# Optimization experiments

Hardware: AMD Instinct MI355X
Metric: run time of the kernel (lower is better)

The kernel has to match this reference:

```python
import jax, jax.numpy as jnp
import numpy as np

ANCHOR_LENGTHS = jnp.array([1., 2., 3., 4., 5., 7., 9.], dtype=jnp.float32)  # A = 7


def make_anchors_1d(Lf):
    # anchors [Lf*A, 2] in feature coords, matching torch make_anchors_1d
    centers = jnp.arange(Lf, dtype=jnp.float32) + 0.5          # [Lf]
    c = centers[:, None]                                        # [Lf,1]
    w = ANCHOR_LENGTHS[None, :]                                 # [1,A]
    start = c - 0.5 * w
    end = c + 0.5 * w
    return jnp.stack(jnp.broadcast_arrays(start, end), axis=-1).reshape(-1, 2)


def setup_inputs() -> dict:
    key = jax.random.key(0)
    ks = jax.random.split(key, 4)
    B, C, Lf, A = 8, 512, 16384, 7
    feat = jax.random.normal(ks[0], (B, C, Lf), dtype=jnp.float32)
    conv_w = jax.random.normal(ks[1], (C, C, 3), dtype=jnp.float32) * 0.02
    conv_b = jnp.zeros((C,), dtype=jnp.float32)
    obj_w = jax.random.normal(ks[2], (A, C, 1), dtype=jnp.float32) * 0.02
    obj_b = jnp.zeros((A,), dtype=jnp.float32)
    reg_w = jax.random.normal(ks[3], (A * 2, C, 1), dtype=jnp.float32) * 0.02
    reg_b = jnp.zeros((A * 2,), dtype=jnp.float32)
    return {"feat": feat, "conv_w": conv_w, "conv_b": conv_b,
            "obj_w": obj_w, "obj_b": obj_b, "reg_w": reg_w, "reg_b": reg_b}


def reference(feat, conv_w, conv_b, obj_w, obj_b, reg_w, reg_b):
    B, C, Lf = feat.shape
    A = obj_w.shape[0]
    # conv1d k=3 pad=1 (NCH layout), + bias, relu
    h = jax.lax.conv_general_dilated(
        feat, conv_w, window_strides=(1,), padding=((1, 1),),
        dimension_numbers=("NCH", "OIH", "NCH"))
    h = jax.nn.relu(h + conv_b[None, :, None])                  # [B,C,Lf]
    # 1x1 heads as channel contractions
    obj = jnp.einsum("bcl,ac->bla", h, obj_w[:, :, 0]) + obj_b  # [B,Lf,A]
    reg = jnp.einsum("bcl,oc->blo", h, reg_w[:, :, 0]) + reg_b  # [B,Lf,2A]
    obj = obj.reshape(B, Lf * A)                                # [B,N]
    reg = reg.reshape(B, Lf, A, 2).reshape(B, Lf * A, 2)        # [B,N,2]
    anchors = make_anchors_1d(Lf)                               # [N,2]
    return obj, reg, anchors
```

## Files before the change

### kernel.cpp

```cpp
#include <hip/hip_runtime.h>
#include <hip/hip_bf16.h>
#include <stdint.h>

typedef __attribute__((ext_vector_type(4))) float f32x4;
typedef unsigned short u16;
typedef unsigned int u32;
typedef unsigned char u8;

#define B_    8
#define C_    512
#define LF    16384
#define KTOT  1536

#define P4_BYTES ((size_t)4 * B_ * 21 * LF * 4)
#define W8_OFF   P4_BYTES

#define OBJ_OFF  0
#define REG_OFF  917504
#define ANC_OFF  2752512

__device__ __forceinline__ u16 f2bf(float f) {
    u32 u = __float_as_uint(f);
    return (u16)((u + 0x7FFFu + ((u >> 16) & 1u)) >> 16);
}
__device__ __forceinline__ u32 pk2bf(float lo, float hi) {
    u32 r;
    asm("v_cvt_pk_bf16_f32 %0, %1, %2" : "=v"(r) : "v"(lo), "v"(hi));
    return r;
}
__device__ __forceinline__ void gload16(const u8* g, u8* l) {
    __builtin_amdgcn_global_load_lds(
        (const __attribute__((address_space(1))) void*)g,
        (__attribute__((address_space(3))) void*)l, 16, 0, 0);
}

__global__ void k_cast_w(const float* __restrict__ cw, u8* __restrict__ W8) {
    int i = blockIdx.x * 256 + threadIdx.x;
    if (i >= C_ * KTOT / 2) return;
    int co = i / (KTOT / 2), r = (i % (KTOT / 2)) * 2;
    int t = r / 512, rem = r % 512;
    int kc = rem >> 6, cc = rem & 63;
    int jl = (cc >> 3) ^ (co & 7);
    int ci = kc * 64 + jl * 8 + (cc & 7);
    float f0 = cw[(co * C_ + ci) * 3 + t];
    float f1 = cw[(co * C_ + ci + 1) * 3 + t];
    u32 pk = __builtin_amdgcn_cvt_pk_fp8_f32(f0, f1, 0, false);
    *(u16*)&W8[(size_t)co * KTOT + r] = (u16)pk;
}

__global__ void k_anchors(float* __restrict__ out) {
    int l = blockIdx.x * 256 + threadIdx.x;
    if (l >= LF) return;
    const float AL[7] = {1.f, 2.f, 3.f, 4.f, 5.f, 7.f, 9.f};
    float c = (float)l + 0.5f;
    float* an = out + ANC_OFF + (size_t)l * 14;
#pragma unroll
    for (int a = 0; a < 7; ++a) {
        an[a * 2 + 0] = c - 0.5f * AL[a];
        an[a * 2 + 1] = c + 0.5f * AL[a];
    }
}

__global__ __launch_bounds__(256, 4) void k_conv_head(
    const float* __restrict__ feat, const u8* __restrict__ W8,
    const float* __restrict__ conv_b, const float* __restrict__ obj_w,
    const float* __restrict__ reg_w, float* __restrict__ P4) {
    __shared__ __align__(16) char smem[40960];
    u8* As3 = (u8*)smem;
    u8* Bs  = (u8*)(smem + 24576);
    u16* Hs = (u16*)smem;
    u16* Wp = (u16*)(smem + 32768);

    const int tid = threadIdx.x;
    const int lane = tid & 63, wave = tid >> 6;
    const int wm = wave >> 1, wn = wave & 1;
    const int g = lane >> 4, cL = lane & 15;

    const int wg = (blockIdx.x & 7) * 512 + (blockIdx.x >> 3);
    const int mt = wg & 3;
    const int l0 = ((wg >> 2) & 127) * 128;
    const int b  = wg >> 9;
    const int co0 = mt * 128;

    const int cg = tid & 15, lgrp = tid >> 4;
    const int swA8 = (cL & 7) << 3;

    f32x4 acc[4][4];
#pragma unroll
    for (int m = 0; m < 4; ++m)
#pragma unroll
        for (int n = 0; n < 4; ++n) acc[m][n] = {0.f, 0.f, 0.f, 0.f};

    for (int kc = 0; kc < 8; ++kc) {
        __syncthreads();
        {
            const float* fp = feat +
                ((size_t)(b * C_ + kc * 64 + cg * 4)) * LF + l0 + lgrp * 8;
#pragma unroll
            for (int h = 0; h < 2; ++h) {
                float4 v0 = *(const float4*)(fp + 0 * LF + h * 4);
                float4 v1 = *(const float4*)(fp + 1 * LF + h * 4);
                float4 v2 = *(const float4*)(fp + 2 * LF + h * 4);
                float4 v3 = *(const float4*)(fp + 3 * LF + h * 4);
#pragma unroll
                for (int e = 0; e < 4; ++e) {
                    const int r = 1 + lgrp * 8 + h * 4 + e;
                    u32 w0 = __builtin_amdgcn_cvt_pk_fp8_f32(
                        ((const float*)&v0)[e], ((const float*)&v1)[e], 0, false);
                    u32 w  = __builtin_amdgcn_cvt_pk_fp8_f32(
                        ((const float*)&v2)[e], ((const float*)&v3)[e], w0, true);
                    *(u32*)&Bs[r * 64 + ((cg * 4) ^ ((r & 7) << 3))] = w;
                }
            }
        }
        if (tid < 128) {
            const int ci2 = tid >> 1;
            const int rr = (tid & 1) ? 129 : 0;
            const int l = l0 + ((tid & 1) ? 128 : -1);
            float v = (l >= 0 && l < LF)
                          ? feat[((size_t)(b * C_ + kc * 64 + ci2)) * LF + l]
                          : 0.f;
            u32 p = __builtin_amdgcn_cvt_pk_fp8_f32(v, 0.f, 0, false);
            Bs[rr * 64 + (ci2 ^ ((rr & 7) << 3))] = (u8)p;
        }
#pragma unroll
        for (int t = 0; t < 3; ++t)
#pragma unroll
            for (int p = 0; p < 2; ++p) {
                const int row = p * 64 + (tid >> 2);
                const int colB = (tid & 3) * 16;
                gload16(&W8[(size_t)(co0 + row) * KTOT + t * 512 + kc * 64 + colB],
                        &As3[t * 8192 + row * 64 + colB]);
            }
        __syncthreads();
#pragma unroll
        for (int t = 0; t < 3; ++t) {
            const u8* At = As3 + t * 8192;
            const int swB8 = ((cL + t) & 7) << 3;
#pragma unroll
            for (int kk = 0; kk < 2; ++kk) {
                const int ko = kk * 32 + g * 8;
                long af[4], bfr[4];
#pragma unroll
                for (int m = 0; m < 4; ++m)
                    af[m] = *(const long*)&At[(wm * 64 + m * 16 + cL) * 64 + (ko ^ swA8)];
#pragma unroll
                for (int n = 0; n < 4; ++n)
                    bfr[n] = *(const long*)&Bs[(wn * 64 + n * 16 + cL + t) * 64 + (ko ^ swB8)];
#pragma unroll
                for (int m = 0; m < 4; ++m)
#pragma unroll
                    for (int n = 0; n < 4; ++n)
                        acc[m][n] = __builtin_amdgcn_mfma_f32_16x16x32_fp8_fp8(
                            af[m], bfr[n], acc[m][n], 0, 0, 0);
            }
        }
    }
    __syncthreads();

#pragma unroll
    for (int m = 0; m < 4; ++m) {
        const int co_b = wm * 64 + m * 16 + g * 4;
        const float b0_ = conv_b[co0 + co_b + 0];
        const float b1_ = conv_b[co0 + co_b + 1];
        const float b2_ = conv_b[co0 + co_b + 2];
        const float b3_ = conv_b[co0 + co_b + 3];
#pragma unroll
        for (int n = 0; n < 4; ++n) {
            const int l = wn * 64 + n * 16 + cL;
            f32x4 v = acc[m][n];
            uint2 pk;
            pk.x = pk2bf(fmaxf(v[0] + b0_, 0.f), fmaxf(v[1] + b1_, 0.f));
            pk.y = pk2bf(fmaxf(v[2] + b2_, 0.f), fmaxf(v[3] + b3_, 0.f));
            *(uint2*)&Hs[l * 128 + (co_b ^ ((cL & 7) << 3))] = pk;
        }
    }
#pragma unroll
    for (int it = 0; it < 4; ++it) {
        const int q = it * 256 + tid;
        const int a = q >> 5, c0 = (q & 31) * 4;
        float4 wv = {0.f, 0.f, 0.f, 0.f};
        if (a < 7)       wv = *(const float4*)&obj_w[a * C_ + co0 + c0];
        else if (a < 21) wv = *(const float4*)&reg_w[(a - 7) * C_ + co0 + c0];
        uint2 pk;
        pk.x = pk2bf(wv.x, wv.y);
        pk.y = pk2bf(wv.z, wv.w);
        *(uint2*)&Wp[a * 128 + (c0 ^ ((a & 7) << 3))] = pk;
    }
    __syncthreads();

    typedef __attribute__((ext_vector_type(8))) short bh8;
    f32x4 hacc[2][2];
#pragma unroll
    for (int m = 0; m < 2; ++m)
#pragma unroll
        for (int n = 0; n < 2; ++n) hacc[m][n] = {0.f, 0.f, 0.f, 0.f};
    const int ln0 = wave * 32;
    const int swA = (cL & 7) << 3;
#pragma unroll
    for (int ks2 = 0; ks2 < 4; ++ks2) {
        const int ko = ks2 * 32 + g * 8;
        bh8 wa[2], hb[2];
        wa[0] = *(const bh8*)&Wp[cL * 128 + (ko ^ swA)];
        wa[1] = *(const bh8*)&Wp[(16 + cL) * 128 + (ko ^ swA)];
        hb[0] = *(const bh8*)&Hs[(ln0 + cL) * 128 + (ko ^ swA)];
        hb[1] = *(const bh8*)&Hs[(ln0 + 16 + cL) * 128 + (ko ^ swA)];
#pragma unroll
        for (int m = 0; m < 2; ++m)
#pragma unroll
            for (int n = 0; n < 2; ++n)
                hacc[m][n] = __builtin_amdgcn_mfma_f32_16x16x32_bf16(
                    wa[m], hb[n], hacc[m][n], 0, 0, 0);
    }
    float* P4base = P4 + ((size_t)(mt * B_ + b) * 21) * LF + l0;
#pragma unroll
    for (int m = 0; m < 2; ++m) {
        const int a0 = m * 16 + g * 4;
#pragma unroll
        for (int n = 0; n < 2; ++n) {
            const int l = ln0 + n * 16 + cL;
#pragma unroll
            for (int r = 0; r < 4; ++r) {
                const int a = a0 + r;
                if (a < 21) P4base[(size_t)a * LF + l] = hacc[m][n][r];
            }
        }
    }
}

__global__ void k_finalize(const float* __restrict__ P4, const float* __restrict__ obj_b,
                           const float* __restrict__ reg_b, float* __restrict__ out) {
    int gid = blockIdx.x * 256 + threadIdx.x;
    if (gid >= B_ * LF) return;
    int b = gid >> 14, l = gid & (LF - 1);
    float s[21];
#pragma unroll
    for (int a = 0; a < 21; ++a) {
        float v = 0.f;
#pragma unroll
        for (int m = 0; m < 4; ++m) v += P4[((size_t)(m * B_ + b) * 21 + a) * LF + l];
        s[a] = v;
    }
    float* op = out + OBJ_OFF + (size_t)b * (LF * 7) + (size_t)l * 7;
#pragma unroll
    for (int a = 0; a < 7; ++a) op[a] = s[a] + obj_b[a];
    float* rp = out + REG_OFF + (size_t)b * (LF * 14) + (size_t)l * 14;
#pragma unroll
    for (int o = 0; o < 14; ++o) rp[o] = s[7 + o] + reg_b[o];
}

extern "C" void kernel_launch(void* const* d_in, const int* in_sizes, int n_in,
                              void* d_out, int out_size, void* d_ws, size_t ws_size,
                              hipStream_t stream) {
    const float* feat   = (const float*)d_in[0];
    const float* conv_w = (const float*)d_in[1];
    const float* conv_b = (const float*)d_in[2];
    const float* obj_w  = (const float*)d_in[3];
    const float* obj_b  = (const float*)d_in[4];
    const float* reg_w  = (const float*)d_in[5];
    const float* reg_b  = (const float*)d_in[6];
    char* ws = (char*)d_ws;
    float* P4 = (float*)ws;
    u8* W8    = (u8*)(ws + W8_OFF);
    float* out = (float*)d_out;

    k_cast_w<<<1536, 256, 0, stream>>>(conv_w, W8);
    k_anchors<<<64, 256, 0, stream>>>(out);
    k_conv_head<<<4096, 256, 0, stream>>>(feat, W8, conv_b, obj_w, reg_w, P4);
    k_finalize<<<(B_ * LF + 255) / 256, 256, 0, stream>>>(P4, obj_b, reg_b, out);
}
```

Baseline: 243.4 us.

## Switch conv GEMM to 32x32x64 scaled FP8 MFMA with new LDS swizzle

```diff
diff --git a/kernel.cpp b/kernel.cpp
--- a/kernel.cpp
+++ b/kernel.cpp
@@ -3,6 +3,10 @@
 #include <stdint.h>
 
 typedef __attribute__((ext_vector_type(4))) float f32x4;
+typedef __attribute__((ext_vector_type(16))) float f32x16;
+typedef __attribute__((ext_vector_type(4))) int i32x4;
+typedef __attribute__((ext_vector_type(8))) int i32x8;
+typedef __attribute__((ext_vector_type(8))) short bh8;
 typedef unsigned short u16;
 typedef unsigned int u32;
 typedef unsigned char u8;
@@ -11,6 +15,7 @@
 #define C_    512
 #define LF    16384
 #define KTOT  1536
+#define SCL   0x7F7F7F7Fu
 
 #define P4_BYTES ((size_t)4 * B_ * 21 * LF * 4)
 #define W8_OFF   P4_BYTES
@@ -37,15 +42,16 @@
 __global__ void k_cast_w(const float* __restrict__ cw, u8* __restrict__ W8) {
     int i = blockIdx.x * 256 + threadIdx.x;
     if (i >= C_ * KTOT / 2) return;
-    int co = i / (KTOT / 2), r = (i % (KTOT / 2)) * 2;
-    int t = r / 512, rem = r % 512;
-    int kc = rem >> 6, cc = rem & 63;
-    int jl = (cc >> 3) ^ (co & 7);
-    int ci = kc * 64 + jl * 8 + (cc & 7);
+    int co = i / (KTOT / 2);
+    int rr = (i % (KTOT / 2)) * 2;
+    int t = rr / 512, q = rr % 512;
+    int kc = q >> 6, cc = q & 63;
+    int jl = (cc >> 4) ^ ((co >> 1) & 3);
+    int ci = kc * 64 + jl * 16 + (cc & 15);
     float f0 = cw[(co * C_ + ci) * 3 + t];
     float f1 = cw[(co * C_ + ci + 1) * 3 + t];
     u32 pk = __builtin_amdgcn_cvt_pk_fp8_f32(f0, f1, 0, false);
-    *(u16*)&W8[(size_t)co * KTOT + r] = (u16)pk;
+    *(u16*)&W8[(size_t)co * KTOT + rr] = (u16)pk;
 }
 
 __global__ void k_anchors(float* __restrict__ out) {
@@ -61,7 +67,7 @@
     }
 }
 
-__global__ __launch_bounds__(256, 4) void k_conv_head(
+__global__ __launch_bounds__(256, 2) void k_conv_head(
     const float* __restrict__ feat, const u8* __restrict__ W8,
     const float* __restrict__ conv_b, const float* __restrict__ obj_w,
     const float* __restrict__ reg_w, float* __restrict__ P4) {
@@ -75,6 +81,7 @@
     const int lane = tid & 63, wave = tid >> 6;
     const int wm = wave >> 1, wn = wave & 1;
     const int g = lane >> 4, cL = lane & 15;
+    const int r32 = lane & 31, hK = lane >> 5;
 
     const int wg = (blockIdx.x & 7) * 512 + (blockIdx.x >> 3);
     const int mt = wg & 3;
@@ -83,19 +90,22 @@
     const int co0 = mt * 128;
 
     const int cg = tid & 15, lgrp = tid >> 4;
-    const int swA8 = (cL & 7) << 3;
-
-    f32x4 acc[4][4];
-#pragma unroll
-    for (int m = 0; m < 4; ++m)
-#pragma unroll
-        for (int n = 0; n < 4; ++n) acc[m][n] = {0.f, 0.f, 0.f, 0.f};
+
+    f32x16 acc[2][2];
+#pragma unroll
+    for (int mi = 0; mi < 2; ++mi)
+#pragma unroll
+        for (int ni = 0; ni < 2; ++ni)
+#pragma unroll
+            for (int r = 0; r < 16; ++r) acc[mi][ni][r] = 0.f;
 
     for (int kc = 0; kc < 8; ++kc) {
         __syncthreads();
         {
             const float* fp = feat +
                 ((size_t)(b * C_ + kc * 64 + cg * 4)) * LF + l0 + lgrp * 8;
+            const int slog = cg >> 2;
+            const int soff = (cg * 4) & 15;
 #pragma unroll
             for (int h = 0; h < 2; ++h) {
                 float4 v0 = *(const float4*)(fp + 0 * LF + h * 4);
@@ -109,7 +119,8 @@
                         ((const float*)&v0)[e], ((const float*)&v1)[e], 0, false);
                     u32 w  = __builtin_amdgcn_cvt_pk_fp8_f32(
                         ((const float*)&v2)[e], ((const float*)&v3)[e], w0, true);
-                    *(u32*)&Bs[r * 64 + ((cg * 4) ^ ((r & 7) << 3))] = w;
+                    const int pc = ((slog ^ ((r >> 1) & 3)) * 16) + soff;
+                    *(u32*)&Bs[r * 64 + pc] = w;
                 }
             }
         }
@@ -121,7 +132,8 @@
                           ? feat[((size_t)(b * C_ + kc * 64 + ci2)) * LF + l]
                           : 0.f;
             u32 p = __builtin_amdgcn_cvt_pk_fp8_f32(v, 0.f, 0, false);
-            Bs[rr * 64 + (ci2 ^ ((rr & 7) << 3))] = (u8)p;
+            const int pc = (((ci2 >> 4) ^ ((rr >> 1) & 3)) * 16) + (ci2 & 15);
+            Bs[rr * 64 + pc] = (u8)p;
         }
 #pragma unroll
         for (int t = 0; t < 3; ++t)
@@ -136,45 +148,54 @@
 #pragma unroll
         for (int t = 0; t < 3; ++t) {
             const u8* At = As3 + t * 8192;
-            const int swB8 = ((cL + t) & 7) << 3;
-#pragma unroll
-            for (int kk = 0; kk < 2; ++kk) {
-                const int ko = kk * 32 + g * 8;
-                long af[4], bfr[4];
-#pragma unroll
-                for (int m = 0; m < 4; ++m)
-                    af[m] = *(const long*)&At[(wm * 64 + m * 16 + cL) * 64 + (ko ^ swA8)];
-#pragma unroll
-                for (int n = 0; n < 4; ++n)
-                    bfr[n] = *(const long*)&Bs[(wn * 64 + n * 16 + cL + t) * 64 + (ko ^ swB8)];
-#pragma unroll
-                for (int m = 0; m < 4; ++m)
-#pragma unroll
-                    for (int n = 0; n < 4; ++n)
-                        acc[m][n] = __builtin_amdgcn_mfma_f32_16x16x32_fp8_fp8(
-                            af[m], bfr[n], acc[m][n], 0, 0, 0);
-            }
+            i32x8 af[2], bf[2];
+#pragma unroll
+            for (int mi = 0; mi < 2; ++mi) {
+                const int row = wm * 64 + mi * 32 + r32;
+                const int x = (row >> 1) & 3;
+                i32x4 a0 = *(const i32x4*)&At[row * 64 + (((2 * hK) ^ x) * 16)];
+                i32x4 a1 = *(const i32x4*)&At[row * 64 + (((2 * hK + 1) ^ x) * 16)];
+                af[mi] = __builtin_shufflevector(a0, a1, 0, 1, 2, 3, 4, 5, 6, 7);
+            }
+#pragma unroll
+            for (int ni = 0; ni < 2; ++ni) {
+                const int row = wn * 64 + ni * 32 + r32 + t;
+                const int x = (row >> 1) & 3;
+                i32x4 b0 = *(const i32x4*)&Bs[row * 64 + (((2 * hK) ^ x) * 16)];
+                i32x4 b1 = *(const i32x4*)&Bs[row * 64 + (((2 * hK + 1) ^ x) * 16)];
+                bf[ni] = __builtin_shufflevector(b0, b1, 0, 1, 2, 3, 4, 5, 6, 7);
+            }
+#pragma unroll
+            for (int mi = 0; mi < 2; ++mi)
+#pragma unroll
+                for (int ni = 0; ni < 2; ++ni)
+                    acc[mi][ni] = __builtin_amdgcn_mfma_scale_f32_32x32x64_f8f6f4(
+                        af[mi], bf[ni], acc[mi][ni], 0, 0, 0, SCL, 0, SCL);
         }
     }
     __syncthreads();
 
 #pragma unroll
-    for (int m = 0; m < 4; ++m) {
-        const int co_b = wm * 64 + m * 16 + g * 4;
-        const float b0_ = conv_b[co0 + co_b + 0];
-        const float b1_ = conv_b[co0 + co_b + 1];
-        const float b2_ = conv_b[co0 + co_b + 2];
-        const float b3_ = conv_b[co0 + co_b + 3];
-#pragma unroll
-        for (int n = 0; n < 4; ++n) {
-            const int l = wn * 64 + n * 16 + cL;
-            f32x4 v = acc[m][n];
-            uint2 pk;
-            pk.x = pk2bf(fmaxf(v[0] + b0_, 0.f), fmaxf(v[1] + b1_, 0.f));
-            pk.y = pk2bf(fmaxf(v[2] + b2_, 0.f), fmaxf(v[3] + b3_, 0.f));
-            *(uint2*)&Hs[l * 128 + (co_b ^ ((cL & 7) << 3))] = pk;
-        }
-    }
+    for (int mi = 0; mi < 2; ++mi)
+#pragma unroll
+        for (int ni = 0; ni < 2; ++ni) {
+            const int l_loc = wn * 64 + ni * 32 + r32;
+            const int xw = (l_loc & 7) << 3;
+#pragma unroll
+            for (int q = 0; q < 4; ++q) {
+                const int cb = wm * 64 + mi * 32 + q * 8 + 4 * hK;
+                const float b0_ = conv_b[co0 + cb + 0];
+                const float b1_ = conv_b[co0 + cb + 1];
+                const float b2_ = conv_b[co0 + cb + 2];
+                const float b3_ = conv_b[co0 + cb + 3];
+                uint2 pk;
+                pk.x = pk2bf(fmaxf(acc[mi][ni][q * 4 + 0] + b0_, 0.f),
+                             fmaxf(acc[mi][ni][q * 4 + 1] + b1_, 0.f));
+                pk.y = pk2bf(fmaxf(acc[mi][ni][q * 4 + 2] + b2_, 0.f),
+                             fmaxf(acc[mi][ni][q * 4 + 3] + b3_, 0.f));
+                *(uint2*)&Hs[l_loc * 128 + (cb ^ xw)] = pk;
+            }
+        }
 #pragma unroll
     for (int it = 0; it < 4; ++it) {
         const int q = it * 256 + tid;
@@ -189,7 +210,6 @@
     }
     __syncthreads();
 
-    typedef __attribute__((ext_vector_type(8))) short bh8;
     f32x4 hacc[2][2];
 #pragma unroll
     for (int m = 0; m < 2; ++m)
```

Measured after the change: 236.7 us. 2.8% less time.
